# Performance work log

Measured on AMD Instinct MI355X. Metric: run time of the kernel, lower is better.

The kernel has to match this reference:

```python
import jax, jax.numpy as jnp
import numpy as np

B, H, W, C = 4, 64, 64, 256
CD = C // 8

def setup_inputs() -> dict:
    key = jax.random.key(0)
    ks = jax.random.split(key, 4)
    x = jax.random.normal(ks[0], (B, H, W, C), dtype=jnp.float32)
    Wf = jax.random.normal(ks[1], (C, CD), dtype=jnp.float32) * (1.0 / np.sqrt(C))
    Wg = jax.random.normal(ks[2], (C, CD), dtype=jnp.float32) * (1.0 / np.sqrt(C))
    Wh = jax.random.normal(ks[3], (C, C), dtype=jnp.float32) * (1.0 / np.sqrt(C))
    bf = jnp.zeros((CD,), dtype=jnp.float32)
    bg = jnp.zeros((CD,), dtype=jnp.float32)
    bh = jnp.zeros((C,), dtype=jnp.float32)
    return {"x": x, "Wf": Wf, "bf": bf, "Wg": Wg, "bg": bg, "Wh": Wh, "bh": bh}

def reference(x, Wf, bf, Wg, bg, Wh, bh):
    b, h, w, c = x.shape
    n = h * w
    xf = x.reshape(b, n, c)                       # [B,N,C]
    f = xf @ Wf + bf                              # [B,N,C/8] (1x1 conv == per-token linear)
    g = xf @ Wg + bg                              # [B,N,C/8]
    hh = xf @ Wh + bh                             # [B,N,C]
    s = jnp.einsum('bnd,bmd->bnm', g, f)          # g @ f^T, unscaled
    attn = jax.nn.softmax(s, axis=-1)             # [B,N,N]
    o = jnp.einsum('bnm,bmc->bnc', attn, hh)      # [B,N,C]
    return x + o.reshape(b, h, w, c)
```

## Files before the change

kernel.cpp:

```cpp
#include <hip/hip_runtime.h>
#include <hip/hip_bf16.h>
#include <stdint.h>

#define NN 4096
#define CC 256
#define DD 32
#define PP 36
#define CHW 17408

typedef short    bf16x8 __attribute__((ext_vector_type(8)));
typedef _Float16 f16x8  __attribute__((ext_vector_type(8)));
typedef float    f32x4  __attribute__((ext_vector_type(4)));

__device__ __forceinline__ unsigned short bf16_rne(float x) {
    union { float f; unsigned int u; } v; v.f = x;
    unsigned int u = v.u;
    return (unsigned short)((u + 0x7FFFu + ((u >> 16) & 1u)) >> 16);
}
__device__ __forceinline__ float bf16f(unsigned short h) {
    union { float f; unsigned int u; } v; v.u = ((unsigned int)h) << 16; return v.f;
}
__device__ __forceinline__ unsigned short f16_bits(float x) {
    union { _Float16 h; unsigned short u; } v; v.h = (_Float16)x;
    return v.u;
}
__device__ __forceinline__ void load_lds16(const unsigned short* g, unsigned short* l) {
    __builtin_amdgcn_global_load_lds(
        (const __attribute__((address_space(1))) unsigned int*)g,
        (__attribute__((address_space(3))) unsigned int*)l, 16, 0, 0);
}

__global__ __launch_bounds__(256) void prep_kernel(
    const float* __restrict__ Wf, const float* __restrict__ Wg,
    const float* __restrict__ Wh, unsigned short* __restrict__ Wst)
{
    int id  = blockIdx.x * 256 + threadIdx.x;
    int ks  = id / 12288;
    int rem = id - ks * 12288;
    int row = rem >> 5;
    int k   = ks * 32 + (rem & 31);
    unsigned short outv;
    if (row < 256) {
        outv = bf16_rne(Wh[(size_t)k * CC + row]);
    } else if (row < 320) {
        int d = row - 256;
        float v = (d < 32) ? Wf[(size_t)k * DD + d] : Wg[(size_t)k * DD + (d - 32)];
        outv = bf16_rne(v);
    } else {
        int d = row - 320;
        float v = (d < 32) ? Wf[(size_t)k * DD + d] : Wg[(size_t)k * DD + (d - 32)];
        unsigned short h = bf16_rne(v);
        outv = bf16_rne(v - bf16f(h));
    }
    Wst[id] = outv;
}

__global__ __launch_bounds__(256, 2) void proj_kernel(
    const float* __restrict__ x,
    const float* __restrict__ bfv, const float* __restrict__ bgv,
    const float* __restrict__ bhv,
    const unsigned short* __restrict__ Wst,
    unsigned short* __restrict__ f16b, unsigned short* __restrict__ g16b,
    unsigned short* __restrict__ hhT)
{
    const int tid  = threadIdx.x;
    const int lane = tid & 63;
    const int wv   = tid >> 6;
    const int col  = lane & 15;
    const int quad = lane >> 4;
    const int tok0 = blockIdx.x * 32;
    const int b    = tok0 >> 12;

    __shared__ __align__(16) unsigned short xh[32 * 272];
    __shared__ __align__(16) unsigned short xl[32 * 272];
    __shared__ __align__(16) unsigned short WT[1920 * 8];

    #pragma unroll
    for (int it = 0; it < 8; ++it) {
        int idx = it * 1024 + tid * 4;
        float4 v = *(const float4*)(x + (size_t)tok0 * CC + idx);
        int tok = idx >> 8, k = idx & 255;
        unsigned short h0 = bf16_rne(v.x), h1 = bf16_rne(v.y),
                       h2 = bf16_rne(v.z), h3 = bf16_rne(v.w);
        uint2 wh_, wl_;
        wh_.x = (unsigned int)h0 | ((unsigned int)h1 << 16);
        wh_.y = (unsigned int)h2 | ((unsigned int)h3 << 16);
        wl_.x = (unsigned int)bf16_rne(v.x - bf16f(h0)) |
                ((unsigned int)bf16_rne(v.y - bf16f(h1)) << 16);
        wl_.y = (unsigned int)bf16_rne(v.z - bf16f(h2)) |
                ((unsigned int)bf16_rne(v.w - bf16f(h3)) << 16);
        *(uint2*)&xh[tok * 272 + k] = wh_;
        *(uint2*)&xl[tok * 272 + k] = wl_;
    }

    f32x4 acc[5][2];
    #pragma unroll
    for (int t = 0; t < 5; ++t) {
        int tl = wv * 5 + t;
        float bias;
        if (tl < 16) bias = bhv[tl * 16 + col];
        else { int fd = (tl - 16) * 16 + col;
               bias = (fd < 32) ? bfv[fd] : bgv[fd - 32]; }
        acc[t][0] = (f32x4){bias, bias, bias, bias};
        acc[t][1] = (f32x4){bias, bias, bias, bias};
    }

    for (int ks = 0; ks < 8; ++ks) {
        for (int t = 0; t < 8; ++t) {
            int i = wv + t * 4;
            if (i >= 30) break;
            int l = i * 64 + lane;
            int row = l / 5, g = l - row * 5;
            const unsigned short* gp = (g < 4)
                ? (Wst + (size_t)ks * 12288 + row * 32 + g * 8)
                : (Wst + (size_t)ks * 12288);
            load_lds16(gp, &WT[i * 512]);
        }
        __syncthreads();

        bf16x8 ah[2], al[2];
        #pragma unroll
        for (int mt = 0; mt < 2; ++mt) {
            ah[mt] = *(const bf16x8*)&xh[(mt * 16 + col) * 272 + ks * 32 + quad * 8];
            al[mt] = *(const bf16x8*)&xl[(mt * 16 + col) * 272 + ks * 32 + quad * 8];
        }

        #pragma unroll
        for (int t = 0; t < 5; ++t) {
            int tl = wv * 5 + t;
            int wrow = (tl < 16) ? (tl * 16 + col) : (256 + (tl - 16) * 16 + col);
            bf16x8 bh = *(const bf16x8*)&WT[wrow * 40 + quad * 8];
            #pragma unroll
            for (int mt = 0; mt < 2; ++mt) {
                acc[t][mt] = __builtin_amdgcn_mfma_f32_16x16x32_bf16(ah[mt], bh, acc[t][mt], 0, 0, 0);
                acc[t][mt] = __builtin_amdgcn_mfma_f32_16x16x32_bf16(al[mt], bh, acc[t][mt], 0, 0, 0);
            }
            if (tl >= 16) {
                bf16x8 bl = *(const bf16x8*)&WT[(wrow + 64) * 40 + quad * 8];
                #pragma unroll
                for (int mt = 0; mt < 2; ++mt)
                    acc[t][mt] = __builtin_amdgcn_mfma_f32_16x16x32_bf16(ah[mt], bl, acc[t][mt], 0, 0, 0);
            }
        }
        __syncthreads();
    }

    const int ks_h = (tok0 & 63) >> 5;
    const int kc   = (tok0 & 4095) >> 6;
    const size_t tbase = ((size_t)(b * 64 + kc)) * CHW;
    #pragma unroll
    for (int t = 0; t < 5; ++t) {
        int tl = wv * 5 + t;
        if (tl < 16) {
            #pragma unroll
            for (int mt = 0; mt < 2; ++mt) {
                int qk = mt * 2 + (quad >> 1);
                int jb = (quad & 1) * 4;
                uint2 w;
                w.x = (unsigned int)bf16_rne(acc[t][mt][0]) | ((unsigned int)bf16_rne(acc[t][mt][1]) << 16);
                w.y = (unsigned int)bf16_rne(acc[t][mt][2]) | ((unsigned int)bf16_rne(acc[t][mt][3]) << 16);
                *(uint2*)&hhT[tbase + (size_t)(((ks_h * 17 + tl) * 64) + qk * 16 + col) * 8 + jb] = w;
            }
        } else {
            int fd = (tl - 16) * 16 + col;
            unsigned short* dst = (fd < 32) ? f16b : g16b;
            int d = fd & 31;
            #pragma unroll
            for (int mt = 0; mt < 2; ++mt)
                #pragma unroll
                for (int r = 0; r < 4; ++r) {
                    int tok = tok0 + mt * 16 + quad * 4 + r;
                    dst[(size_t)tok * DD + d] = f16_bits(acc[t][mt][r]);
                }
        }
    }
    #pragma unroll
    for (int it = 0; it < 2; ++it) {
        int e = tid + it * 256;
        int j = e & 7, ck = (e >> 3) & 15, qk = e >> 7;
        hhT[tbase + (size_t)(((ks_h * 17 + 16) * 64) + qk * 16 + ck) * 8 + j] =
            (ck == 0) ? (unsigned short)0x3F80 : (unsigned short)0;
    }
}

__global__ __launch_bounds__(256, 2) void attn_kernel(
    const unsigned short* __restrict__ g16b,
    const unsigned short* __restrict__ f16b,
    const unsigned short* __restrict__ hhT,
    float* __restrict__ O0,
    float* __restrict__ O1, float* __restrict__ O2, float* __restrict__ O3,
    float* __restrict__ lbuf)
{
    const int tid  = threadIdx.x;
    const int lane = tid & 63;
    const int wv   = tid >> 6;
    const int col  = lane & 15;
    const int quad = lane >> 4;
    const int bid  = blockIdx.x;
    const int sp   = bid & 3;
    const int b    = (bid >> 2) & 3;
    const int qblk = bid >> 4;
    const int q0   = qblk * 128 + wv * 32;
    const int kcb  = sp * 16;

    __shared__ __align__(16) unsigned short hbuf[2][CHW];
    __shared__ __align__(8)  unsigned short p_all[4][32 * PP];
    unsigned short* p_lds = p_all[wv];

    const unsigned short* fb16 = f16b + (size_t)b * NN * DD;
    const unsigned short* hb   = hhT + (size_t)b * 64 * CHW;

    f16x8 a_g[2];
    #pragma unroll
    for (int a = 0; a < 2; ++a)
        a_g[a] = *(const f16x8*)(g16b + ((size_t)(b * NN + q0 + a * 16 + col)) * DD + quad * 8);

    f32x4 zero = {0.f, 0.f, 0.f, 0.f};
    f32x4 acc[2][17];
    #pragma unroll
    for (int a = 0; a < 2; ++a)
        #pragma unroll
        for (int i = 0; i < 17; ++i) acc[a][i] = zero;

    {
        const unsigned short* tile = hb + (size_t)kcb * CHW;
        for (int t = 0; t < 9; ++t) {
            int i = wv + t * 4;
            if (i >= 34) break;
            load_lds16(tile + (size_t)(i * 64 + lane) * 8, &hbuf[0][i * 512]);
        }
    }
    __syncthreads();

    for (int kc = 0; kc < 16; ++kc) {
        const int nb  = kc & 1;
        const int kk0 = (kcb + kc) * 64;

        if (kc + 1 < 16) {
            const unsigned short* tile = hb + (size_t)(kcb + kc + 1) * CHW;
            for (int t = 0; t < 9; ++t) {
                int i = wv + t * 4;
                if (i >= 34) break;
                load_lds16(tile + (size_t)(i * 64 + lane) * 8, &hbuf[nb ^ 1][i * 512]);
            }
        }

        #pragma unroll
        for (int half = 0; half < 2; ++half) {
            f32x4 s_t[2][2];
            #pragma unroll
            for (int ktl = 0; ktl < 2; ++ktl) {
                f16x8 bf_ = *(const f16x8*)(fb16 +
                    (size_t)(kk0 + half * 32 + ktl * 16 + col) * DD + quad * 8);
                #pragma unroll
                for (int a = 0; a < 2; ++a)
                    s_t[ktl][a] = __builtin_amdgcn_mfma_f32_16x16x32_f16(a_g[a], bf_, zero, 0, 0, 0);
            }

            #pragma unroll
            for (int ktl = 0; ktl < 2; ++ktl)
                #pragma unroll
                for (int a = 0; a < 2; ++a) {
                    unsigned short pv[4];
                    #pragma unroll
                    for (int r = 0; r < 4; ++r)
                        pv[r] = bf16_rne(__expf(s_t[ktl][a][r] - 40.0f));
                    uint2 w2;
                    w2.x = (unsigned int)pv[0] | ((unsigned int)pv[1] << 16);
                    w2.y = (unsigned int)pv[2] | ((unsigned int)pv[3] << 16);
                    *(uint2*)&p_lds[(ktl * 16 + col) * PP + a * 16 + quad * 4] = w2;
                }

            bf16x8 a_p[2];
            #pragma unroll
            for (int a = 0; a < 2; ++a)
                #pragma unroll
                for (int j = 0; j < 8; ++j)
                    a_p[a][j] = (short)p_lds[(quad * 8 + j) * PP + a * 16 + col];

            #pragma unroll
            for (int ct = 0; ct < 17; ++ct) {
                bf16x8 bh = *(const bf16x8*)&hbuf[nb][(size_t)(((half * 17 + ct) * 64) + lane) * 8];
                acc[0][ct] = __builtin_amdgcn_mfma_f32_16x16x32_bf16(a_p[0], bh, acc[0][ct], 0, 0, 0);
                acc[1][ct] = __builtin_amdgcn_mfma_f32_16x16x32_bf16(a_p[1], bh, acc[1][ct], 0, 0, 0);
            }
        }

        __syncthreads();
    }

    float* Ops[4] = {O0, O1, O2, O3};
    float* Op = Ops[sp];
    #pragma unroll
    for (int a = 0; a < 2; ++a) {
        const size_t obase = (size_t)(b * NN + q0 + a * 16) * CC;
        #pragma unroll
        for (int ct = 0; ct < 16; ++ct) {
            #pragma unroll
            for (int r = 0; r < 4; ++r)
                Op[obase + (size_t)(quad * 4 + r) * CC + ct * 16 + col] = acc[a][ct][r];
        }
        if (col == 0) {
            #pragma unroll
            for (int r = 0; r < 4; ++r)
                lbuf[sp * (4 * NN) + b * NN + q0 + a * 16 + quad * 4 + r] = acc[a][16][r];
        }
    }
}

__global__ __launch_bounds__(256) void reduce_kernel(
    const float* __restrict__ x,
    const float* __restrict__ O1, const float* __restrict__ O2,
    const float* __restrict__ O3,
    const float* __restrict__ lbuf, float* __restrict__ out)
{
    int id = blockIdx.x * 256 + threadIdx.x;
    int q  = id >> 6;
    int c4 = (id & 63) * 4;
    size_t base = (size_t)q * CC + c4;
    float inv = 1.0f / (lbuf[q] + lbuf[4 * NN + q] + lbuf[8 * NN + q] + lbuf[12 * NN + q]);
    float4 o0 = *(const float4*)(out + base);
    float4 o1 = *(const float4*)(O1 + base);
    float4 o2 = *(const float4*)(O2 + base);
    float4 o3 = *(const float4*)(O3 + base);
    float4 xv = *(const float4*)(x + base);
    float4 r;
    r.x = xv.x + (o0.x + o1.x + o2.x + o3.x) * inv;
    r.y = xv.y + (o0.y + o1.y + o2.y + o3.y) * inv;
    r.z = xv.z + (o0.z + o1.z + o2.z + o3.z) * inv;
    r.w = xv.w + (o0.w + o1.w + o2.w + o3.w) * inv;
    *(float4*)(out + base) = r;
}

extern "C" void kernel_launch(void* const* d_in, const int* in_sizes, int n_in,
                              void* d_out, int out_size, void* d_ws, size_t ws_size,
                              hipStream_t stream) {
    const float* x  = (const float*)d_in[0];
    const float* Wf = (const float*)d_in[1];
    const float* bf = (const float*)d_in[2];
    const float* Wg = (const float*)d_in[3];
    const float* bg = (const float*)d_in[4];
    const float* Wh = (const float*)d_in[5];
    const float* bh = (const float*)d_in[6];
    float* out = (float*)d_out;

    unsigned char* ws = (unsigned char*)d_ws;
    unsigned short* Wst  = (unsigned short*)(ws);
    unsigned short* f16b = (unsigned short*)(ws + 0x040000);
    unsigned short* g16b = (unsigned short*)(ws + 0x140000);
    unsigned short* hhT  = (unsigned short*)(ws + 0x240000);
    float*          O1   = (float*)(ws + 0xAC0000);
    float*          O2   = (float*)(ws + 0x1AC0000);
    float*          O3   = (float*)(ws + 0x2AC0000);
    float*          lbuf = (float*)(ws + 0x3AC0000);

    prep_kernel<<<384, 256, 0, stream>>>(Wf, Wg, Wh, Wst);
    proj_kernel<<<512, 256, 0, stream>>>(x, bf, bg, bh, Wst, f16b, g16b, hhT);
    attn_kernel<<<512, 256, 0, stream>>>(g16b, f16b, hhT, out, O1, O2, O3, lbuf);
    reduce_kernel<<<4096, 256, 0, stream>>>(x, O1, O2, O3, lbuf, out);
}
```

Before: 155.4 us.

## Split attention output channels across two blocks to raise occupancy

Each attention block now covers half of the 256 value channels (8 tiles plus the row-sum tile) rather than all of them, which doubles the grid to 1024 blocks. Accumulator registers and the LDS value buffer shrink to match, so launch bounds allow 4 blocks per CU. The key loop now runs over 32-key half-chunks with its own double buffering. In exchange, the QK^T MFMAs and the exp work are computed twice, once in each channel half.

After: 170.5 us. 1.1x slower.

```diff
diff --git a/kernel.cpp b/kernel.cpp
--- a/kernel.cpp
+++ b/kernel.cpp
@@ -7,6 +7,7 @@
 #define DD 32
 #define PP 36
 #define CHW 17408
+#define NCT 9
 
 typedef short    bf16x8 __attribute__((ext_vector_type(8)));
 typedef _Float16 f16x8  __attribute__((ext_vector_type(8)));
@@ -183,7 +184,7 @@
     }
 }
 
-__global__ __launch_bounds__(256, 2) void attn_kernel(
+__global__ __launch_bounds__(256, 4) void attn_kernel(
     const unsigned short* __restrict__ g16b,
     const unsigned short* __restrict__ f16b,
     const unsigned short* __restrict__ hhT,
@@ -197,13 +198,14 @@
     const int col  = lane & 15;
     const int quad = lane >> 4;
     const int bid  = blockIdx.x;
-    const int sp   = bid & 3;
-    const int b    = (bid >> 2) & 3;
-    const int qblk = bid >> 4;
+    const int csp  = bid & 1;
+    const int sp   = (bid >> 1) & 3;
+    const int b    = (bid >> 3) & 3;
+    const int qblk = bid >> 5;
     const int q0   = qblk * 128 + wv * 32;
     const int kcb  = sp * 16;
 
-    __shared__ __align__(16) unsigned short hbuf[2][CHW];
+    __shared__ __align__(16) unsigned short hbuf[2][NCT * 512];
     __shared__ __align__(8)  unsigned short p_all[4][32 * PP];
     unsigned short* p_lds = p_all[wv];
 
@@ -216,74 +218,78 @@
         a_g[a] = *(const f16x8*)(g16b + ((size_t)(b * NN + q0 + a * 16 + col)) * DD + quad * 8);
 
     f32x4 zero = {0.f, 0.f, 0.f, 0.f};
-    f32x4 acc[2][17];
+    f32x4 acc[2][NCT];
     #pragma unroll
     for (int a = 0; a < 2; ++a)
         #pragma unroll
-        for (int i = 0; i < 17; ++i) acc[a][i] = zero;
+        for (int i = 0; i < NCT; ++i) acc[a][i] = zero;
 
     {
         const unsigned short* tile = hb + (size_t)kcb * CHW;
-        for (int t = 0; t < 9; ++t) {
-            int i = wv + t * 4;
-            if (i >= 34) break;
-            load_lds16(tile + (size_t)(i * 64 + lane) * 8, &hbuf[0][i * 512]);
+        #pragma unroll
+        for (int t = 0; t < 3; ++t) {
+            int s = wv + t * 4;
+            if (s >= NCT) break;
+            int ct = (s < 8) ? (csp * 8 + s) : 16;
+            load_lds16(tile + (size_t)ct * 512 + lane * 8, &hbuf[0][s * 512]);
         }
     }
     __syncthreads();
 
-    for (int kc = 0; kc < 16; ++kc) {
-        const int nb  = kc & 1;
-        const int kk0 = (kcb + kc) * 64;
-
-        if (kc + 1 < 16) {
-            const unsigned short* tile = hb + (size_t)(kcb + kc + 1) * CHW;
-            for (int t = 0; t < 9; ++t) {
-                int i = wv + t * 4;
-                if (i >= 34) break;
-                load_lds16(tile + (size_t)(i * 64 + lane) * 8, &hbuf[nb ^ 1][i * 512]);
-            }
-        }
-
-        #pragma unroll
-        for (int half = 0; half < 2; ++half) {
-            f32x4 s_t[2][2];
-            #pragma unroll
-            for (int ktl = 0; ktl < 2; ++ktl) {
-                f16x8 bf_ = *(const f16x8*)(fb16 +
-                    (size_t)(kk0 + half * 32 + ktl * 16 + col) * DD + quad * 8);
+    for (int hs = 0; hs < 32; ++hs) {
+        const int nb = hs & 1;
+
+        if (hs + 1 < 32) {
+            const int kc = kcb + ((hs + 1) >> 1);
+            const int ks = (hs + 1) & 1;
+            const unsigned short* tile = hb + (size_t)kc * CHW + (size_t)(ks * 17) * 512;
+            #pragma unroll
+            for (int t = 0; t < 3; ++t) {
+                int s = wv + t * 4;
+                if (s >= NCT) break;
+                int ct = (s < 8) ? (csp * 8 + s) : 16;
+                load_lds16(tile + (size_t)ct * 512 + lane * 8, &hbuf[nb ^ 1][s * 512]);
+            }
+        }
+
+        const int kk0 = kcb * 64 + hs * 32;
+
+        f32x4 s_t[2][2];
+        #pragma unroll
+        for (int ktl = 0; ktl < 2; ++ktl) {
+            f16x8 bf_ = *(const f16x8*)(fb16 +
+                (size_t)(kk0 + ktl * 16 + col) * DD + quad * 8);
+            #pragma unroll
+            for (int a = 0; a < 2; ++a)
+                s_t[ktl][a] = __builtin_amdgcn_mfma_f32_16x16x32_f16(a_g[a], bf_, zero, 0, 0, 0);
+        }
+
+        #pragma unroll
+        for (int ktl = 0; ktl < 2; ++ktl)
+            #pragma unroll
+            for (int a = 0; a < 2; ++a) {
+                unsigned short pv[4];
                 #pragma unroll
-                for (int a = 0; a < 2; ++a)
-                    s_t[ktl][a] = __builtin_amdgcn_mfma_f32_16x16x32_f16(a_g[a], bf_, zero, 0, 0, 0);
-            }
-
-            #pragma unroll
-            for (int ktl = 0; ktl < 2; ++ktl)
-                #pragma unroll
-                for (int a = 0; a < 2; ++a) {
-                    unsigned short pv[4];
-                    #pragma unroll
-                    for (int r = 0; r < 4; ++r)
-                        pv[r] = bf16_rne(__expf(s_t[ktl][a][r] - 40.0f));
-                    uint2 w2;
-                    w2.x = (unsigned int)pv[0] | ((unsigned int)pv[1] << 16);
-                    w2.y = (unsigned int)pv[2] | ((unsigned int)pv[3] << 16);
-                    *(uint2*)&p_lds[(ktl * 16 + col) * PP + a * 16 + quad * 4] = w2;
-                }
-
-            bf16x8 a_p[2];
-            #pragma unroll
-            for (int a = 0; a < 2; ++a)
-                #pragma unroll
-                for (int j = 0; j < 8; ++j)
-                    a_p[a][j] = (short)p_lds[(quad * 8 + j) * PP + a * 16 + col];
-
-            #pragma unroll
-            for (int ct = 0; ct < 17; ++ct) {
-                bf16x8 bh = *(const bf16x8*)&hbuf[nb][(size_t)(((half * 17 + ct) * 64) + lane) * 8];
-                acc[0][ct] = __builtin_amdgcn_mfma_f32_16x16x32_bf16(a_p[0], bh, acc[0][ct], 0, 0, 0);
-                acc[1][ct] = __builtin_amdgcn_mfma_f32_16x16x32_bf16(a_p[1], bh, acc[1][ct], 0, 0, 0);
-            }
+                for (int r = 0; r < 4; ++r)
+                    pv[r] = bf16_rne(__expf(s_t[ktl][a][r] - 40.0f));
+                uint2 w2;
+                w2.x = (unsigned int)pv[0] | ((unsigned int)pv[1] << 16);
+                w2.y = (unsigned int)pv[2] | ((unsigned int)pv[3] << 16);
+                *(uint2*)&p_lds[(ktl * 16 + col) * PP + a * 16 + quad * 4] = w2;
+            }
+
+        bf16x8 a_p[2];
+        #pragma unroll
+        for (int a = 0; a < 2; ++a)
+            #pragma unroll
+            for (int j = 0; j < 8; ++j)
+                a_p[a][j] = (short)p_lds[(quad * 8 + j) * PP + a * 16 + col];
+
+        #pragma unroll
+        for (int s = 0; s < NCT; ++s) {
+            bf16x8 bh = *(const bf16x8*)&hbuf[nb][(s * 64 + lane) * 8];
+            acc[0][s] = __builtin_amdgcn_mfma_f32_16x16x32_bf16(a_p[0], bh, acc[0][s], 0, 0, 0);
+            acc[1][s] = __builtin_amdgcn_mfma_f32_16x16x32_bf16(a_p[1], bh, acc[1][s], 0, 0, 0);
         }
 
         __syncthreads();
@@ -295,15 +301,16 @@
     for (int a = 0; a < 2; ++a) {
         const size_t obase = (size_t)(b * NN + q0 + a * 16) * CC;
         #pragma unroll
-        for (int ct = 0; ct < 16; ++ct) {
+        for (int s = 0; s < 8; ++s) {
+            const int ch = (csp * 8 + s) * 16 + col;
             #pragma unroll
             for (int r = 0; r < 4; ++r)
-                Op[obase + (size_t)(quad * 4 + r) * CC + ct * 16 + col] = acc[a][ct][r];
-        }
-        if (col == 0) {
+                Op[obase + (size_t)(quad * 4 + r) * CC + ch] = acc[a][s][r];
+        }
+        if (csp == 0 && col == 0) {
             #pragma unroll
             for (int r = 0; r < 4; ++r)
-                lbuf[sp * (4 * NN) + b * NN + q0 + a * 16 + quad * 4 + r] = acc[a][16][r];
+                lbuf[sp * (4 * NN) + b * NN + q0 + a * 16 + quad * 4 + r] = acc[a][8][r];
         }
     }
 }
@@ -356,6 +363,6 @@
 
     prep_kernel<<<384, 256, 0, stream>>>(Wf, Wg, Wh, Wst);
     proj_kernel<<<512, 256, 0, stream>>>(x, bf, bg, bh, Wst, f16b, g16b, hhT);
-    attn_kernel<<<512, 256, 0, stream>>>(g16b, f16b, hhT, out, O1, O2, O3, lbuf);
+    attn_kernel<<<1024, 256, 0, stream>>>(g16b, f16b, hhT, out, O1, O2, O3, lbuf);
     reduce_kernel<<<4096, 256, 0, stream>>>(x, O1, O2, O3, lbuf, out);
 }
```
